# Performance work log

Hardware: AMD Instinct MI355X
Metric: run time of the kernel (lower is better)

## Reference

```python
import jax, jax.numpy as jnp
import numpy as np

N, E, F, D, G, K = 50000, 1600000, 128, 256, 64, 10


def setup_inputs() -> dict:
    key = jax.random.key(0)
    ks = jax.random.split(key, 20)
    x = jax.random.normal(ks[0], (N, F), dtype=jnp.float32)
    edge_index = jax.random.randint(ks[1], (2, E), 0, N, dtype=jnp.int64)
    batch_index = jnp.sort(jax.random.randint(ks[2], (N,), 0, G, dtype=jnp.int64))

    def lin(k, fan_in, fan_out):
        w = jax.random.normal(k, (fan_in, fan_out), dtype=jnp.float32) / np.sqrt(fan_in)
        return w

    return {
        "x": x, "edge_index": edge_index, "batch_index": batch_index,
        "W0": lin(ks[3], F, D), "b0": jnp.zeros((D,), jnp.float32),
        "W1": lin(ks[4], D, D), "b1": jnp.zeros((D,), jnp.float32),
        "W2": lin(ks[5], D, D), "b2": jnp.zeros((D,), jnp.float32),
        "W3": lin(ks[6], D, D), "b3": jnp.zeros((D,), jnp.float32),
        "fc1_w": lin(ks[7], 2 * D, 512), "fc1_b": jnp.zeros((512,), jnp.float32),
        "fc2_w": lin(ks[8], 512, 256), "fc2_b": jnp.zeros((256,), jnp.float32),
        "out_w": lin(ks[9], 256, K), "out_b": jnp.zeros((K,), jnp.float32),
    }


def _gcn_conv(x, W, b, src, dst, dis):
    # PyG GCNConv: h = x W; out = D^{-1/2}(A+I)D^{-1/2} h + b  (self-loops added)
    h = x @ W                                   # [N, D]
    norm = dis[src] * dis[dst]                  # [E]
    msg = h[src] * norm[:, None]                # [E, D]
    agg = jax.ops.segment_sum(msg, dst, num_segments=x.shape[0])
    agg = agg + h * (dis * dis)[:, None]        # self-loop contribution
    return agg + b


def reference(x, edge_index, batch_index, W0, b0, W1, b1, W2, b2, W3, b3,
              fc1_w, fc1_b, fc2_w, fc2_b, out_w, out_b):
    src, dst = edge_index[0], edge_index[1]
    n = x.shape[0]
    # degree with self-loops
    deg = 1.0 + jax.ops.segment_sum(jnp.ones((src.shape[0],), jnp.float32), dst,
                                    num_segments=n)
    dis = jax.lax.rsqrt(deg)

    h = jnp.tanh(_gcn_conv(x, W0, b0, src, dst, dis))
    h = jnp.tanh(_gcn_conv(h, W1, b1, src, dst, dis))
    h = jnp.tanh(_gcn_conv(h, W2, b2, src, dst, dis))
    h = jnp.tanh(_gcn_conv(h, W3, b3, src, dst, dis))

    # global max pool + global mean pool over graphs in the batch
    gmax = jax.ops.segment_max(h, batch_index, num_segments=G)
    gsum = jax.ops.segment_sum(h, batch_index, num_segments=G)
    cnt = jax.ops.segment_sum(jnp.ones((n,), jnp.float32), batch_index,
                              num_segments=G)
    gmean = gsum / jnp.maximum(cnt, 1.0)[:, None]
    g = jnp.concatenate([gmax, gmean], axis=1)  # [G, 2D]

    g = jax.nn.relu(g @ fc1_w + fc1_b)
    g = jax.nn.relu(g @ fc2_w + fc2_b)
    return g @ out_w + out_b
```

## Files before the change

kernel.cpp:

```cpp
#include <hip/hip_runtime.h>
#include <hip/hip_bf16.h>


#define NNODES 50000
#define DDIM 256
#define NBUCK 196
#define BCAP 16384
#define CHUNK_AB 6400
#define NGRAPH 64
#define PCHUNK 8

typedef __attribute__((ext_vector_type(8))) short short8;
typedef __attribute__((ext_vector_type(4))) float float4_;
typedef __attribute__((ext_vector_type(2))) float float2_;

__device__ __forceinline__ float fast_tanh(float x) {
    float e = __expf(2.0f * x);
    return 1.0f - 2.0f / (e + 1.0f);
}

__device__ __forceinline__ float bf2f(unsigned short u) {
    return __uint_as_float(((unsigned)u) << 16);
}
__device__ __forceinline__ unsigned short f2bf(float f) {
    unsigned u = __float_as_uint(f);
    u = u + 0x7fffu + ((u >> 16) & 1u);
    return (unsigned short)(u >> 16);
}

__global__ void build_partition(const int* __restrict__ ei, int* __restrict__ bcnt,
                                unsigned* __restrict__ pairs, int E) {
    __shared__ int hist[NBUCK];
    __shared__ int base[NBUCK];
    __shared__ int cursor[NBUCK];
    int t = threadIdx.x;
    int e0 = blockIdx.x * CHUNK_AB;
    int lim = E - e0;
    if (lim > CHUNK_AB) lim = CHUNK_AB;
    if (t < NBUCK) { hist[t] = 0; cursor[t] = 0; }
    __syncthreads();
    for (int i = t; i < lim; i += 256)
        atomicAdd(&hist[ei[E + e0 + i] >> 8], 1);
    __syncthreads();
    if (t < NBUCK) {
        int h = hist[t];
        base[t] = h ? atomicAdd(&bcnt[t], h) : 0;
    }
    __syncthreads();
    for (int i = t; i < lim; i += 256) {
        int dst = ei[E + e0 + i];
        int src = ei[e0 + i];
        int b = dst >> 8;
        int r = atomicAdd(&cursor[b], 1);
        pairs[(size_t)b * BCAP + base[b] + r] =
            ((unsigned)(dst & 255) << 16) | (unsigned)src;
    }
}

__global__ void build_csr(const unsigned* __restrict__ pairs, const int* __restrict__ bcnt,
                          int* __restrict__ deg, int* __restrict__ rowptr,
                          float* __restrict__ dis, unsigned short* __restrict__ col, int N) {
    __shared__ int sc[256];
    __shared__ int hist[256];
    __shared__ int cursor[256];
    int b = blockIdx.x;
    int t = threadIdx.x;
    sc[t] = (t < NBUCK) ? bcnt[t] : 0;
    __syncthreads();
    for (int off = 1; off < 256; off <<= 1) {
        int v = (t >= off) ? sc[t - off] : 0;
        __syncthreads();
        sc[t] += v;
        __syncthreads();
    }
    int bstart = (b == 0) ? 0 : sc[b - 1];
    int cnt = bcnt[b];
    __syncthreads();
    hist[t] = 0; cursor[t] = 0;
    __syncthreads();
    const unsigned* bp = pairs + (size_t)b * BCAP;
    for (int i = t; i < cnt; i += 256)
        atomicAdd(&hist[bp[i] >> 16], 1);
    __syncthreads();
    sc[t] = hist[t];
    __syncthreads();
    for (int off = 1; off < 256; off <<= 1) {
        int v = (t >= off) ? sc[t - off] : 0;
        __syncthreads();
        sc[t] += v;
        __syncthreads();
    }
    int n = b * 256 + t;
    if (n < N) {
        int d = hist[t];
        deg[n] = d;
        dis[n] = rsqrtf(1.0f + (float)d);
        rowptr[n] = bstart + sc[t] - d;
    }
    __syncthreads();
    for (int i = t; i < cnt; i += 256) {
        unsigned p = bp[i];
        int low = p >> 16;
        int r = atomicAdd(&cursor[low], 1);
        col[bstart + (sc[low] - hist[low]) + r] = (unsigned short)(p & 0xffffu);
    }
}

#define CAST_BLOCKS ((NNODES * 128) / 256)
__global__ void prep_kernel(const float* __restrict__ x, const float* __restrict__ dis,
                            unsigned short* __restrict__ xh,
                            const float* __restrict__ W0, const float* __restrict__ W1,
                            const float* __restrict__ W2, const float* __restrict__ W3,
                            unsigned short* __restrict__ wt0, unsigned short* __restrict__ wt1,
                            unsigned short* __restrict__ wt2, unsigned short* __restrict__ wt3) {
    int b = blockIdx.x;
    int t = threadIdx.x;
    if (b < CAST_BLOCKS) {
        int i = b * 256 + t;
        xh[i] = f2bf(x[i] * dis[i >> 7]);
        return;
    }
    b -= CAST_BLOCKS;
    const float* W; unsigned short* Wt; int K; int k;
    if (b < 128)      { W = W0; Wt = wt0; K = 128; k = b; }
    else if (b < 384) { W = W1; Wt = wt1; K = 256; k = b - 128; }
    else if (b < 640) { W = W2; Wt = wt2; K = 256; k = b - 384; }
    else              { W = W3; Wt = wt3; K = 256; k = b - 640; }
    Wt[t * K + k] = f2bf(W[k * 256 + t]);
}

__device__ __forceinline__ void paddu(float2_* acc, uint4 u) {
    float2_ v0 = {__uint_as_float(u.x << 16), __uint_as_float(u.x & 0xffff0000u)};
    float2_ v1 = {__uint_as_float(u.y << 16), __uint_as_float(u.y & 0xffff0000u)};
    float2_ v2 = {__uint_as_float(u.z << 16), __uint_as_float(u.z & 0xffff0000u)};
    float2_ v3 = {__uint_as_float(u.w << 16), __uint_as_float(u.w & 0xffff0000u)};
    acc[0] += v0; acc[1] += v1; acc[2] += v2; acc[3] += v3;
}
__device__ __forceinline__ void paddw(float2_* acc, uint4 u, float w) {
    float2_ w2 = {w, w};
    float2_ v0 = {__uint_as_float(u.x << 16), __uint_as_float(u.x & 0xffff0000u)};
    float2_ v1 = {__uint_as_float(u.y << 16), __uint_as_float(u.y & 0xffff0000u)};
    float2_ v2 = {__uint_as_float(u.z << 16), __uint_as_float(u.z & 0xffff0000u)};
    float2_ v3 = {__uint_as_float(u.w << 16), __uint_as_float(u.w & 0xffff0000u)};
    acc[0] += v0 * w2; acc[1] += v1 * w2; acc[2] += v2 * w2; acc[3] += v3 * w2;
}

template <int W, int S, bool FINALIZE>
__global__ void msgpass_bf16(const unsigned short* __restrict__ in,
                             unsigned short* __restrict__ out,
                             const int* __restrict__ rowptr, const int* __restrict__ deg,
                             const unsigned short* __restrict__ col,
                             const float* __restrict__ dis, const float* __restrict__ bias) {
    constexpr int L = W / 8;
    constexpr int P = 64 / L;
    int lane = threadIdx.x & 63;
    int wav  = threadIdx.x >> 6;
    int n = blockIdx.x * 4 + wav;
    if (n >= NNODES) return;
    int part = lane / L;
    int sl   = lane % L;
    int start = rowptr[n];
    int cnt   = deg[n];
    float dn = dis[n];
    const uint4* inb = (const uint4*)in + sl;
    float2_ acc[4];
#pragma unroll
    for (int j = 0; j < 4; ++j) { float2_ z = {0.0f, 0.0f}; acc[j] = z; }

    int e = 0;
    for (; e + 8 * P <= cnt; e += 8 * P) {
        int c[8];
        uint4 u[8];
#pragma unroll
        for (int q = 0; q < 8; ++q)
            c[q] = col[start + e + q * P + part];
#pragma unroll
        for (int q = 0; q < 8; ++q)
            u[q] = *(inb + (size_t)c[q] * (S / 8));
#pragma unroll
        for (int q = 0; q < 8; ++q)
            paddu(acc, u[q]);
    }
    for (; e + 4 * P <= cnt; e += 4 * P) {
        int c0 = col[start + e + part];
        int c1 = col[start + e + P + part];
        int c2 = col[start + e + 2 * P + part];
        int c3 = col[start + e + 3 * P + part];
        uint4 u0 = *(inb + (size_t)c0 * (S / 8));
        uint4 u1 = *(inb + (size_t)c1 * (S / 8));
        uint4 u2 = *(inb + (size_t)c2 * (S / 8));
        uint4 u3 = *(inb + (size_t)c3 * (S / 8));
        paddu(acc, u0);
        paddu(acc, u1);
        paddu(acc, u2);
        paddu(acc, u3);
    }
    for (; e + P <= cnt; e += P) {
        int c = col[start + e + part];
        uint4 u = *(inb + (size_t)c * (S / 8));
        paddu(acc, u);
    }
    int r = cnt - e;
    if (r > 0) {
        int c = (part < r) ? (int)col[start + e + part] : n;
        float w = (part < r) ? 1.0f : 0.0f;
        uint4 u = *(inb + (size_t)c * (S / 8));
        paddw(acc, u, w);
    }
    {
        float w = (part == 0) ? 1.0f : 0.0f;
        uint4 u = *(inb + (size_t)n * (S / 8));
        paddw(acc, u, w);
    }
#pragma unroll
    for (int j = 0; j < 4; ++j) {
#pragma unroll
        for (int h = 0; h < 2; ++h) {
            if (P == 4) acc[j][h] += __shfl(acc[j][h], lane ^ 16);
            acc[j][h] += __shfl(acc[j][h], lane ^ 32);
        }
    }
    if (part == 0) {
        float a[8] = {acc[0][0], acc[0][1], acc[1][0], acc[1][1],
                      acc[2][0], acc[2][1], acc[3][0], acc[3][1]};
        if (FINALIZE) {
#pragma unroll
            for (int j = 0; j < 8; ++j)
                a[j] = fast_tanh(fmaf(a[j], dn, bias[sl * 8 + j]));
        } else {
#pragma unroll
            for (int j = 0; j < 8; ++j)
                a[j] *= dn;
        }
        uint4 o;
        o.x = (unsigned)f2bf(a[0]) | ((unsigned)f2bf(a[1]) << 16);
        o.y = (unsigned)f2bf(a[2]) | ((unsigned)f2bf(a[3]) << 16);
        o.z = (unsigned)f2bf(a[4]) | ((unsigned)f2bf(a[5]) << 16);
        o.w = (unsigned)f2bf(a[6]) | ((unsigned)f2bf(a[7]) << 16);
        *((uint4*)(out + (size_t)n * S) + sl) = o;
    }
}

template <int K, bool TANH>
__launch_bounds__(256, 2)
__global__ void gemm_mfma(const short* __restrict__ A, const short* __restrict__ Bt,
                          const float* __restrict__ bias, const float* __restrict__ dis,
                          unsigned short* __restrict__ C, int N) {
    constexpr int PK = 72;
    __shared__ __align__(16) short As[128 * PK];
    __shared__ __align__(16) short Bs[128 * PK];
    int t = threadIdx.x;
    int lane = t & 63;
    int w    = t >> 6;
    int wr = w & 1;
    int wc = w >> 1;
    int m0 = blockIdx.x * 128;
    int n0 = blockIdx.y * 128;

    int srow = t >> 2;
    int koff = (t & 3) * 8;
    int arow0 = m0 + srow;      if (arow0 > N - 1) arow0 = N - 1;
    int arow1 = m0 + 64 + srow; if (arow1 > N - 1) arow1 = N - 1;
    const short8* ap0 = (const short8*)(A + (size_t)arow0 * K + koff);
    const short8* ap1 = (const short8*)(A + (size_t)arow1 * K + koff);
    const short8* bp0 = (const short8*)(Bt + (size_t)(n0 + srow) * K + koff);
    const short8* bp1 = (const short8*)(Bt + (size_t)(n0 + 64 + srow) * K + koff);

    float4_ acc[4][4];
#pragma unroll
    for (int i = 0; i < 4; ++i)
#pragma unroll
        for (int j = 0; j < 4; ++j) {
            float4_ z = {0.0f, 0.0f, 0.0f, 0.0f};
            acc[i][j] = z;
        }

    constexpr int NKB = K / 64;
    int g = lane >> 4;
    int r = lane & 15;

    short8 a00 = ap0[0], a01 = ap0[4];
    short8 a10 = ap1[0], a11 = ap1[4];
    short8 b00 = bp0[0], b01 = bp0[4];
    short8 b10 = bp1[0], b11 = bp1[4];

    for (int kb = 0; kb < NKB; ++kb) {
        __syncthreads();
        *(short8*)&As[srow * PK + koff]             = a00;
        *(short8*)&As[srow * PK + koff + 32]        = a01;
        *(short8*)&As[(64 + srow) * PK + koff]      = a10;
        *(short8*)&As[(64 + srow) * PK + koff + 32] = a11;
        *(short8*)&Bs[srow * PK + koff]             = b00;
        *(short8*)&Bs[srow * PK + koff + 32]        = b01;
        *(short8*)&Bs[(64 + srow) * PK + koff]      = b10;
        *(short8*)&Bs[(64 + srow) * PK + koff + 32] = b11;
        __syncthreads();
        if (kb + 1 < NKB) {
            int o = (kb + 1) * 8;
            a00 = ap0[o]; a01 = ap0[o + 4];
            a10 = ap1[o]; a11 = ap1[o + 4];
            b00 = bp0[o]; b01 = bp0[o + 4];
            b10 = bp1[o]; b11 = bp1[o + 4];
        }
#pragma unroll
        for (int s = 0; s < 2; ++s) {
            short8 af[4], bfr[4];
#pragma unroll
            for (int i = 0; i < 4; ++i)
                af[i] = *(const short8*)&As[(wr * 64 + i * 16 + r) * PK + s * 32 + g * 8];
#pragma unroll
            for (int j = 0; j < 4; ++j)
                bfr[j] = *(const short8*)&Bs[(wc * 64 + j * 16 + r) * PK + s * 32 + g * 8];
#pragma unroll
            for (int i = 0; i < 4; ++i)
#pragma unroll
                for (int j = 0; j < 4; ++j)
                    acc[i][j] = __builtin_amdgcn_mfma_f32_16x16x32_bf16(af[i], bfr[j],
                                                                        acc[i][j], 0, 0, 0);
        }
    }

#pragma unroll
    for (int i = 0; i < 4; ++i) {
        int rowb = m0 + wr * 64 + i * 16 + g * 4;
#pragma unroll
        for (int rr = 0; rr < 4; ++rr) {
            int row = rowb + rr;
            if (row < N) {
                float dsc = TANH ? 0.0f : dis[row];
#pragma unroll
                for (int j = 0; j < 4; ++j) {
                    int cb = n0 + wc * 64 + j * 16 + r;
                    float v = acc[i][j][rr];
                    if (TANH) v = fast_tanh(v + bias[cb]);
                    else      v = v * dsc;
                    C[(size_t)row * 256 + cb] = f2bf(v);
                }
            }
        }
    }
}

__global__ void pool_kernel(const unsigned short* __restrict__ act,
                            const int* __restrict__ batch,
                            float* __restrict__ psum, float* __restrict__ pmax,
                            int* __restrict__ gcnt, int N) {
    int g = blockIdx.x >> 3;
    int c = blockIdx.x & 7;
    int t = threadIdx.x;
    __shared__ int bounds[2];
    if (t < 2) {
        int target = g + t;
        int lo = 0, hi = N;
        while (lo < hi) {
            int m = (lo + hi) >> 1;
            if (batch[m] < target) lo = m + 1; else hi = m;
        }
        bounds[t] = lo;
    }
    __syncthreads();
    int s = bounds[0];
    int e = bounds[1];
    int len = e - s;
    if (len < 0) len = 0;
    if (c == 0 && t == 0) gcnt[g] = len;
    int n0 = s + (int)(((long long)len * c) >> 3);
    int n1 = s + (int)(((long long)len * (c + 1)) >> 3);
    float sum = 0.0f, mx = -2.0f;
    int n = n0;
    for (; n + 4 <= n1; n += 4) {
        float v0 = bf2f(act[(size_t)(n + 0) * DDIM + t]);
        float v1 = bf2f(act[(size_t)(n + 1) * DDIM + t]);
        float v2 = bf2f(act[(size_t)(n + 2) * DDIM + t]);
        float v3 = bf2f(act[(size_t)(n + 3) * DDIM + t]);
        sum += (v0 + v1) + (v2 + v3);
        mx = fmaxf(fmaxf(mx, v0), fmaxf(fmaxf(v1, v2), v3));
    }
    for (; n < n1; ++n) {
        float v = bf2f(act[(size_t)n * DDIM + t]);
        sum += v;
        mx = fmaxf(mx, v);
    }
    psum[(size_t)blockIdx.x * DDIM + t] = sum;
    pmax[(size_t)blockIdx.x * DDIM + t] = mx;
}

__launch_bounds__(1024, 1)
__global__ void mlp_kernel(const float* __restrict__ psum, const float* __restrict__ pmax,
                           const int* __restrict__ gcnt,
                           const float* __restrict__ fc1_w, const float* __restrict__ fc1_b,
                           const float* __restrict__ fc2_w, const float* __restrict__ fc2_b,
                           const float* __restrict__ out_w, const float* __restrict__ out_b,
                           float* __restrict__ out) {
    int g = blockIdx.x;
    int t = threadIdx.x;
    __shared__ float gv[512];
    __shared__ float t1[512];
    __shared__ float t2[256];
    __shared__ float ps[2][512];
    __shared__ float ps2[4][256];
    __shared__ float pso[32][16];
    if (t < 512) {
        if (t < 256) {
            float m = pmax[(size_t)(g * PCHUNK) * DDIM + t];
#pragma unroll
            for (int c = 1; c < PCHUNK; ++c)
                m = fmaxf(m, pmax[(size_t)(g * PCHUNK + c) * DDIM + t]);
            gv[t] = m;
        } else {
            int tt = t - 256;
            float sm = 0.0f;
#pragma unroll
            for (int c = 0; c < PCHUNK; ++c)
                sm += psum[(size_t)(g * PCHUNK + c) * DDIM + tt];
            float cnt = fmaxf((float)gcnt[g], 1.0f);
            gv[t] = sm / cnt;
        }
    }
    __syncthreads();
    {
        int j = t & 511;
        int h = t >> 9;
        float a = 0.0f;
        const float* wp = fc1_w + (size_t)(h * 256) * 512 + j;
#pragma unroll 8
        for (int k = 0; k < 256; ++k)
            a = fmaf(gv[h * 256 + k], wp[(size_t)k * 512], a);
        ps[h][j] = a;
    }
    __syncthreads();
    if (t < 512)
        t1[t] = fmaxf(ps[0][t] + ps[1][t] + fc1_b[t], 0.0f);
    __syncthreads();
    {
        int j = t & 255;
        int h = t >> 8;
        float a = 0.0f;
        const float* wp = fc2_w + (size_t)(h * 128) * 256 + j;
#pragma unroll 8
        for (int k = 0; k < 128; ++k)
            a = fmaf(t1[h * 128 + k], wp[(size_t)k * 256], a);
        ps2[h][j] = a;
    }
    __syncthreads();
    if (t < 256)
        t2[t] = fmaxf(ps2[0][t] + ps2[1][t] + ps2[2][t] + ps2[3][t] + fc2_b[t], 0.0f);
    __syncthreads();
    if (t < 512) {
        int j = t & 15;
        int h = t >> 4;
        float a = 0.0f;
        if (j < 10) {
#pragma unroll
            for (int k = 0; k < 8; ++k)
                a = fmaf(t2[h * 8 + k], out_w[(size_t)(h * 8 + k) * 10 + j], a);
        }
        pso[h][j] = a;
    }
    __syncthreads();
    if (t < 10) {
        float o = out_b[t];
#pragma unroll
        for (int h = 0; h < 32; ++h)
            o += pso[h][t];
        out[g * 10 + t] = o;
    }
}

extern "C" void kernel_launch(void* const* d_in, const int* in_sizes, int n_in,
                              void* d_out, int out_size, void* d_ws, size_t ws_size,
                              hipStream_t stream) {
    const float* x      = (const float*)d_in[0];
    const int*   ei     = (const int*)d_in[1];
    const int*   batch  = (const int*)d_in[2];
    const float* W0     = (const float*)d_in[3];
    const float* b0     = (const float*)d_in[4];
    const float* W1     = (const float*)d_in[5];
    const float* b1     = (const float*)d_in[6];
    const float* W2     = (const float*)d_in[7];
    const float* b2     = (const float*)d_in[8];
    const float* W3     = (const float*)d_in[9];
    const float* b3     = (const float*)d_in[10];
    const float* fc1_w  = (const float*)d_in[11];
    const float* fc1_b  = (const float*)d_in[12];
    const float* fc2_w  = (const float*)d_in[13];
    const float* fc2_b  = (const float*)d_in[14];
    const float* out_w  = (const float*)d_in[15];
    const float* out_b  = (const float*)d_in[16];
    float* out = (float*)d_out;

    const int N = in_sizes[2];
    const int E = in_sizes[1] / 2;

    char* ws = (char*)d_ws;
    const size_t off_deg    = 0;
    const size_t off_gcnt   = 331264;
    const size_t off_dis    = 331776;
    const size_t off_rowptr = 531968;
    const size_t off_bcnt   = 732160;
    const size_t off_col    = 932352;
    const size_t off_xh     = 7332352;
    const size_t off_wt0    = 20132352;
    const size_t off_wt1    = 20197888;
    const size_t off_wt2    = 20328960;
    const size_t off_wt3    = 20460032;
    const size_t off_bufA   = 20591104;
    const size_t off_bufB   = 46191104;

    int*            deg    = (int*)(ws + off_deg);
    int*            gcnt   = (int*)(ws + off_gcnt);
    float*          dis    = (float*)(ws + off_dis);
    int*            rowptr = (int*)(ws + off_rowptr);
    int*            bcnt   = (int*)(ws + off_bcnt);
    unsigned short* col    = (unsigned short*)(ws + off_col);
    unsigned short* xh     = (unsigned short*)(ws + off_xh);
    short*          wt0    = (short*)(ws + off_wt0);
    short*          wt1    = (short*)(ws + off_wt1);
    short*          wt2    = (short*)(ws + off_wt2);
    short*          wt3    = (short*)(ws + off_wt3);
    unsigned short* bufA   = (unsigned short*)(ws + off_bufA);
    unsigned short* bufB   = (unsigned short*)(ws + off_bufB);
    unsigned*       pairs  = (unsigned*)(ws + off_bufA);
    float*          psum   = (float*)(ws + off_xh);
    float*          pmax   = (float*)(ws + off_xh + 524288);

    hipMemsetAsync(ws + off_bcnt, 0, 1024, stream);

    build_partition<<<(E + CHUNK_AB - 1) / CHUNK_AB, 256, 0, stream>>>(ei, bcnt, pairs, E);
    build_csr<<<NBUCK, 256, 0, stream>>>(pairs, bcnt, deg, rowptr, dis, col, N);

    prep_kernel<<<CAST_BLOCKS + 896, 256, 0, stream>>>(
        x, dis, xh, W0, W1, W2, W3,
        (unsigned short*)wt0, (unsigned short*)wt1,
        (unsigned short*)wt2, (unsigned short*)wt3);

    msgpass_bf16<128, 128, false><<<(N + 3) / 4, 256, 0, stream>>>(
        xh, bufB, rowptr, deg, col, dis, nullptr);
    gemm_mfma<128, true><<<dim3((N + 127) / 128, 2), 256, 0, stream>>>(
        (const short*)bufB, wt0, b0, dis, bufA, N);

    const short* wts[3] = {wt1, wt2, wt3};
    const float* bs_[3] = {b1, b2, b3};
    for (int l = 0; l < 3; ++l) {
        gemm_mfma<256, false><<<dim3((N + 127) / 128, 2), 256, 0, stream>>>(
            (const short*)bufA, wts[l], nullptr, dis, bufB, N);
        msgpass_bf16<128, 256, true><<<(N + 3) / 4, 256, 0, stream>>>(
            bufB, bufA, rowptr, deg, col, dis, bs_[l]);
        msgpass_bf16<128, 256, true><<<(N + 3) / 4, 256, 0, stream>>>(
            bufB + 128, bufA + 128, rowptr, deg, col, dis, bs_[l] + 128);
    }

    pool_kernel<<<NGRAPH * PCHUNK, 256, 0, stream>>>(bufA, batch, psum, pmax, gcnt, N);
    mlp_kernel<<<NGRAPH, 1024, 0, stream>>>(psum, pmax, gcnt, fc1_w, fc1_b, fc2_w, fc2_b,
                                            out_w, out_b, out);
}
```

Before: 609.6 us.

## Stage GEMM epilogue through LDS for coalesced stores; merge split msgpass launches

```diff
diff --git a/kernel.cpp b/kernel.cpp
--- a/kernel.cpp
+++ b/kernel.cpp
@@ -247,8 +247,10 @@
                           const float* __restrict__ bias, const float* __restrict__ dis,
                           unsigned short* __restrict__ C, int N) {
     constexpr int PK = 72;
-    __shared__ __align__(16) short As[128 * PK];
-    __shared__ __align__(16) short Bs[128 * PK];
+    constexpr int TS = 132;
+    __shared__ __align__(16) short smem[2 * 128 * PK];
+    short* As = smem;
+    short* Bs = smem + 128 * PK;
     int t = threadIdx.x;
     int lane = t & 63;
     int w    = t >> 6;
@@ -320,23 +322,41 @@
         }
     }
 
+    __syncthreads();
+    short* T = smem;
 #pragma unroll
     for (int i = 0; i < 4; ++i) {
-        int rowb = m0 + wr * 64 + i * 16 + g * 4;
-#pragma unroll
-        for (int rr = 0; rr < 4; ++rr) {
-            int row = rowb + rr;
-            if (row < N) {
-                float dsc = TANH ? 0.0f : dis[row];
-#pragma unroll
-                for (int j = 0; j < 4; ++j) {
-                    int cb = n0 + wc * 64 + j * 16 + r;
-                    float v = acc[i][j][rr];
-                    if (TANH) v = fast_tanh(v + bias[cb]);
-                    else      v = v * dsc;
-                    C[(size_t)row * 256 + cb] = f2bf(v);
-                }
+        int lr0 = wr * 64 + i * 16 + g * 4;
+        int grow = m0 + lr0;
+        float d0 = TANH ? 0.0f : dis[(grow + 0 < N) ? grow + 0 : N - 1];
+        float d1 = TANH ? 0.0f : dis[(grow + 1 < N) ? grow + 1 : N - 1];
+        float d2 = TANH ? 0.0f : dis[(grow + 2 < N) ? grow + 2 : N - 1];
+        float d3 = TANH ? 0.0f : dis[(grow + 3 < N) ? grow + 3 : N - 1];
+        float dd[4] = {d0, d1, d2, d3};
+#pragma unroll
+        for (int j = 0; j < 4; ++j) {
+            int lcol = wc * 64 + j * 16 + r;
+            float bb = TANH ? bias[n0 + lcol] : 0.0f;
+#pragma unroll
+            for (int rr = 0; rr < 4; ++rr) {
+                float v = acc[i][j][rr];
+                if (TANH) v = fast_tanh(v + bb);
+                else      v = v * dd[rr];
+                T[(lr0 + rr) * TS + lcol] = (short)f2bf(v);
             }
+        }
+    }
+    __syncthreads();
+    {
+        int row = t >> 1;
+        int h   = t & 1;
+        int grow = m0 + row;
+        if (grow < N) {
+            const short* src = &T[row * TS + h * 64];
+            uint4* dstp = (uint4*)(C + (size_t)grow * 256 + n0 + h * 64);
+#pragma unroll
+            for (int k = 0; k < 8; ++k)
+                dstp[k] = *(const uint4*)(src + k * 8);
         }
     }
 }
@@ -544,10 +564,8 @@
     for (int l = 0; l < 3; ++l) {
         gemm_mfma<256, false><<<dim3((N + 127) / 128, 2), 256, 0, stream>>>(
             (const short*)bufA, wts[l], nullptr, dis, bufB, N);
-        msgpass_bf16<128, 256, true><<<(N + 3) / 4, 256, 0, stream>>>(
+        msgpass_bf16<256, 256, true><<<(N + 3) / 4, 256, 0, stream>>>(
             bufB, bufA, rowptr, deg, col, dis, bs_[l]);
-        msgpass_bf16<128, 256, true><<<(N + 3) / 4, 256, 0, stream>>>(
-            bufB + 128, bufA + 128, rowptr, deg, col, dis, bs_[l] + 128);
     }
 
     pool_kernel<<<NGRAPH * PCHUNK, 256, 0, stream>>>(bufA, batch, psum, pmax, gcnt, N);
```

Measured after the change: 640.9 us. 5.1% more time.
